# Optimization experiments

Hardware: AMD Instinct MI355X
Metric: run time of the kernel (lower is better)

## Reference

```python
import jax, jax.numpy as jnp
import numpy as np

B, T, C = 4, 2048, 1024


def wkv(k, v, w, u, reverse):
    """RWKV WKV scan with running-max stabilization.
    k, v: [B, T, C]; w, u: [C]. Returns y: [B, T, C]."""
    def step(carry, kv):
        num, den, mx = carry          # each [B, C]
        k_t, v_t = kv                 # each [B, C]
        ku = k_t + u
        m = jnp.maximum(mx, ku)
        e1 = jnp.exp(mx - m)
        e2 = jnp.exp(ku - m)
        y = (e1 * num + e2 * v_t) / (e1 * den + e2)
        # state update with decay w
        mw = mx + w
        mn = jnp.maximum(mw, k_t)
        e1s = jnp.exp(mw - mn)
        e2s = jnp.exp(k_t - mn)
        return (e1s * num + e2s * v_t, e1s * den + e2s, mn), y

    z = jnp.zeros_like(k[:, 0])
    init = (z, z, jnp.full_like(z, -1e38))
    ks = jnp.swapaxes(k, 0, 1)  # [T, B, C]
    vs = jnp.swapaxes(v, 0, 1)
    _, ys = jax.lax.scan(step, init, (ks, vs), reverse=reverse)
    return jnp.swapaxes(ys, 0, 1)


def setup_inputs() -> dict:
    key = jax.random.key(0)
    k1, k2, k3, k4, k5, k6, k7 = jax.random.split(key, 7)
    x = jax.random.normal(k1, (B, T, C), dtype=jnp.float32)
    rkv_w = jax.random.normal(k2, (6 * C, C), dtype=jnp.float32) / np.sqrt(C)
    out_w = jax.random.normal(k3, (C, 2 * C), dtype=jnp.float32) / np.sqrt(2 * C)
    time_decay = jax.random.uniform(k4, (C,), jnp.float32, -6.0, -5.0)
    time_first = jax.random.uniform(k5, (C,), jnp.float32, -3.0, 0.0)
    time_decay_rev = jax.random.uniform(k6, (C,), jnp.float32, -6.0, -5.0)
    time_first_rev = jax.random.uniform(k7, (C,), jnp.float32, -3.0, 0.0)
    return {"x": x, "rkv_w": rkv_w, "out_w": out_w,
            "time_decay": time_decay, "time_first": time_first,
            "time_decay_rev": time_decay_rev, "time_first_rev": time_first_rev}


def reference(x, rkv_w, out_w, time_decay, time_first, time_decay_rev, time_first_rev):
    b, t, c = x.shape
    rkv = jnp.einsum('btc,dc->btd', x, rkv_w).reshape(b, t, 2, 3, c)
    r_f, k_f, v_f = rkv[:, :, 0, 0], rkv[:, :, 0, 1], rkv[:, :, 0, 2]
    r_b, k_b, v_b = rkv[:, :, 1, 0], rkv[:, :, 1, 1], rkv[:, :, 1, 2]
    out_f = jax.nn.sigmoid(r_f) * wkv(k_f, v_f, -jnp.exp(time_decay), time_first, False)
    out_b = jax.nn.sigmoid(r_b) * wkv(k_b, v_b, -jnp.exp(time_decay_rev), time_first_rev, True)
    out_cat = jnp.concatenate([out_f, out_b], axis=-1)  # [B, T, 2C]
    return jnp.einsum('btd,cd->btc', out_cat, out_w)
```

## Files before the change

kernel.cpp:

```cpp
#include <hip/hip_runtime.h>
#include <cstdint>
#include <cstddef>

#define Bdim 4
#define Tdim 2048
#define Cdim 1024

#define SEG  64
#define LSEG (Tdim / SEG)

#define G1_K   1024
#define G1_N   6144
#define G1_NKT 32
#define G1_NWG 1536

typedef __attribute__((ext_vector_type(8))) short bf16x8;
typedef __attribute__((ext_vector_type(4))) float f32x4;

__device__ __forceinline__ unsigned short f2bf(float f) {
    unsigned int u = __float_as_uint(f);
    u += 0x7fffu + ((u >> 16) & 1u);
    return (unsigned short)(u >> 16);
}
__device__ __forceinline__ float bf2f(unsigned short h) {
    return __uint_as_float((unsigned int)h << 16);
}
__device__ __forceinline__ float bf2f_lo(unsigned int u) {
    return __uint_as_float(u << 16);
}
__device__ __forceinline__ float bf2f_hi(unsigned int u) {
    return __uint_as_float(u & 0xffff0000u);
}
__device__ __forceinline__ float frcp(float x) {
    return __builtin_amdgcn_rcpf(x);
}

__device__ __forceinline__ void gload_lds16(const void* g, void* l) {
    __builtin_amdgcn_global_load_lds(
        (const __attribute__((address_space(1))) unsigned int*)g,
        (__attribute__((address_space(3))) unsigned int*)l,
        16, 0, 0);
}

__global__ __launch_bounds__(256) void cast_all(
    const float* __restrict__ x,  unsigned short* __restrict__ xb,  int n1,
    const float* __restrict__ w1, unsigned short* __restrict__ wb,  int n2,
    const float* __restrict__ w2, unsigned short* __restrict__ ob,  int n3)
{
    int i = blockIdx.x * 256 + threadIdx.x;
    const float* in; unsigned short* out;
    if (i < n1)           { in = x;  out = xb; }
    else if (i < n1 + n2) { in = w1; out = wb; i -= n1; }
    else if (i < n1 + n2 + n3) { in = w2; out = ob; i -= n1 + n2; }
    else return;
    float4 v = ((const float4*)in)[i];
    ushort4 o;
    o.x = f2bf(v.x); o.y = f2bf(v.y); o.z = f2bf(v.z); o.w = f2bf(v.w);
    ((ushort4*)out)[i] = o;
}

__device__ __forceinline__ void stage_128(
    const unsigned short* __restrict__ G, int row0, int K, int elemoff,
    char* slot, int wave, int lane)
{
    const int sl = (lane & 3) ^ ((lane >> 3) & 3);
    const unsigned short* gp = G + (size_t)(row0 + wave * 16 + (lane >> 2)) * K
                                 + elemoff + sl * 8;
    gload_lds16(gp, slot + wave * 1024);
}

__global__ __launch_bounds__(512, 4) void gemm1_3slot(
    const unsigned short* __restrict__ A, const unsigned short* __restrict__ B,
    unsigned short* __restrict__ C)
{
    __shared__ char ldsb[73728];

    const int tid  = threadIdx.x;
    const int wave = tid >> 6;
    const int lane = tid & 63;
    const int wm = wave >> 1;
    const int wn = wave & 1;
    const int fr = lane & 15;
    const int cswz = (((lane >> 4) ^ ((fr >> 1) & 3)) << 4);

    const int xcd = blockIdx.x & 7;
    const int li  = blockIdx.x >> 3;
    const int bx  = li >> 2;
    const int by  = xcd * 4 + (li & 3);
    const int m0 = by * 256;
    const int n0 = bx * 128;

    f32x4 acc[4][4] = {};

    stage_128(A, m0,       G1_K, 0,  ldsb + 0,            wave, lane);
    stage_128(A, m0 + 128, G1_K, 0,  ldsb + 8192,         wave, lane);
    stage_128(B, n0,       G1_K, 0,  ldsb + 49152,        wave, lane);
    stage_128(A, m0,       G1_K, 32, ldsb + 16384,        wave, lane);
    stage_128(A, m0 + 128, G1_K, 32, ldsb + 16384 + 8192, wave, lane);
    stage_128(B, n0,       G1_K, 32, ldsb + 49152 + 8192, wave, lane);
    asm volatile("s_waitcnt vmcnt(3)" ::: "memory");
    __builtin_amdgcn_s_barrier();
    __builtin_amdgcn_sched_barrier(0);

    int sR = 0;
    for (int t = 0; t < G1_NKT; ++t) {
        const int sW = (sR >= 1) ? sR - 1 : 2;
        int kst = t + 2; if (kst > G1_NKT - 1) kst = G1_NKT - 1;
        const int keoff = kst * 32;

        const char* Asl = ldsb + sR * 16384;
        const char* Bsl = ldsb + 49152 + sR * 8192;

        bf16x8 af[4], bq[4];
        #pragma unroll
        for (int i_ = 0; i_ < 4; ++i_)
            af[i_] = *(const bf16x8*)(Asl + (wm * 64 + i_ * 16 + fr) * 64 + cswz);
        #pragma unroll
        for (int j_ = 0; j_ < 4; ++j_)
            bq[j_] = *(const bf16x8*)(Bsl + (wn * 64 + j_ * 16 + fr) * 64 + cswz);

        stage_128(A, m0,       G1_K, keoff, ldsb + sW * 16384,        wave, lane);
        stage_128(A, m0 + 128, G1_K, keoff, ldsb + sW * 16384 + 8192, wave, lane);
        stage_128(B, n0,       G1_K, keoff, ldsb + 49152 + sW * 8192, wave, lane);

        __builtin_amdgcn_s_barrier();
        __builtin_amdgcn_sched_barrier(0);
        __builtin_amdgcn_s_setprio(1);
        #pragma unroll
        for (int i_ = 0; i_ < 4; ++i_)
            #pragma unroll
            for (int j_ = 0; j_ < 4; ++j_)
                acc[i_][j_] = __builtin_amdgcn_mfma_f32_16x16x32_bf16(
                    af[i_], bq[j_], acc[i_][j_], 0, 0, 0);
        __builtin_amdgcn_s_setprio(0);
        asm volatile("s_waitcnt vmcnt(3)" ::: "memory");
        __builtin_amdgcn_s_barrier();
        __builtin_amdgcn_sched_barrier(0);

        sR = (sR < 2) ? sR + 1 : 0;
    }

    #pragma unroll
    for (int i_ = 0; i_ < 4; ++i_) {
        const int row = m0 + wm * 64 + i_ * 16 + (lane >> 4) * 4;
        #pragma unroll
        for (int j_ = 0; j_ < 4; ++j_) {
            const int col = n0 + wn * 64 + j_ * 16 + fr;
            #pragma unroll
            for (int r = 0; r < 4; ++r)
                C[(size_t)(row + r) * G1_N + col] = f2bf(acc[i_][j_][r]);
        }
    }
}

__global__ __launch_bounds__(256) void gemm_bf16_nt(
    const unsigned short* __restrict__ A, const unsigned short* __restrict__ B,
    float* __restrict__ C, int M, int N, int K)
{
    __shared__ unsigned short As[128 * 32];
    __shared__ unsigned short Bs[128 * 32];

    const int tid  = threadIdx.x;
    const int wave = tid >> 6;
    const int lane = tid & 63;
    const int m0 = blockIdx.y * 128;
    const int n0 = blockIdx.x * 128;
    const int wr = wave >> 1, wc = wave & 1;

    const int srow = tid >> 2;
    const int scol = (tid & 3) * 8;
    const unsigned short* Ag = A + (size_t)(m0 + srow) * K + scol;
    const unsigned short* Bg = B + (size_t)(n0 + srow) * K + scol;
    char* AsW = (char*)As + wave * 1024;
    char* BsW = (char*)Bs + wave * 1024;

    f32x4 acc[4][4] = {};

    const int fr = lane & 15;
    const int fk = (lane >> 4) * 8;

    for (int k0 = 0; k0 < K; k0 += 32) {
        gload_lds16(Ag + k0,                  AsW);
        gload_lds16(Ag + k0 + (size_t)64 * K, AsW + 4096);
        gload_lds16(Bg + k0,                  BsW);
        gload_lds16(Bg + k0 + (size_t)64 * K, BsW + 4096);
        __syncthreads();

        bf16x8 af[4], bfr_[4];
        #pragma unroll
        for (int f = 0; f < 4; ++f) {
            af[f]   = *(const bf16x8*)&As[(wr * 64 + f * 16 + fr) * 32 + fk];
            bfr_[f] = *(const bf16x8*)&Bs[(wc * 64 + f * 16 + fr) * 32 + fk];
        }
        #pragma unroll
        for (int i = 0; i < 4; ++i)
            #pragma unroll
            for (int j = 0; j < 4; ++j)
                acc[i][j] = __builtin_amdgcn_mfma_f32_16x16x32_bf16(
                    af[i], bfr_[j], acc[i][j], 0, 0, 0);
        __syncthreads();
    }

    #pragma unroll
    for (int i = 0; i < 4; ++i) {
        const int row = m0 + wr * 64 + i * 16 + (lane >> 4) * 4;
        #pragma unroll
        for (int j = 0; j < 4; ++j) {
            const int col = n0 + wc * 64 + j * 16 + (lane & 15);
            #pragma unroll
            for (int r = 0; r < 4; ++r)
                C[(size_t)(row + r) * N + col] = acc[i][j][r];
        }
    }
}

__global__ __launch_bounds__(1024) void wkv_scan_par(
    const unsigned short* __restrict__ rkv,
    const float* __restrict__ td,  const float* __restrict__ tf,
    const float* __restrict__ tdr, const float* __restrict__ tfr,
    unsigned short* __restrict__ outcat)
{
    __shared__ float sBn[SEG][32], sBd[SEG][32], sMb[SEG][32];

    const int tid = threadIdx.x;
    const int chg = tid & 15;
    const int seg = tid >> 4;

    const int bi  = blockIdx.x;
    const int b   = bi >> 6;
    const int rem = bi & 63;
    const int dir = rem >> 5;
    const int cbase = (rem & 31) * 32;
    const int c0  = cbase + chg * 2;

    const float w0 = -__expf(dir ? tdr[c0]     : td[c0]);
    const float w1 = -__expf(dir ? tdr[c0 + 1] : td[c0 + 1]);
    const float u0 = dir ? tfr[c0]     : tf[c0];
    const float u1 = dir ? tfr[c0 + 1] : tf[c0 + 1];

    const int strideT = 6 * Cdim;
    const int tstep   = dir ? -strideT : strideT;
    const int t0      = dir ? (Tdim - 1 - seg * LSEG) : (seg * LSEG);

    const unsigned short* pbase = rkv + ((size_t)b * Tdim + t0) * strideT + dir * 3 * Cdim + c0;

    const int PF = 8;

    float bn0 = 0.f, bd0 = 0.f, mb0 = -1e38f;
    float bn1 = 0.f, bd1 = 0.f, mb1 = -1e38f;
    {
        const unsigned short* q = pbase;
        unsigned int kk[PF], vv[PF];
        #pragma unroll
        for (int i = 0; i < PF; ++i) {
            kk[i] = *(const unsigned int*)(q + Cdim);
            vv[i] = *(const unsigned int*)(q + 2 * Cdim);
            q += tstep;
        }
        for (int t = 0; t < LSEG; t += PF) {
            unsigned int kn[PF], vn[PF];
            if (t + PF < LSEG) {
                #pragma unroll
                for (int i = 0; i < PF; ++i) {
                    kn[i] = *(const unsigned int*)(q + Cdim);
                    vn[i] = *(const unsigned int*)(q + 2 * Cdim);
                    q += tstep;
                }
            }
            #pragma unroll
            for (int i = 0; i < PF; ++i) {
                {
                    const float k_ = bf2f_lo(kk[i]), v_ = bf2f_lo(vv[i]);
                    const float mw = mb0 + w0;
                    const float mn = fmaxf(mw, k_);
                    const float e1 = __expf(mw - mn);
                    const float e2 = __expf(k_ - mn);
                    bn0 = e1 * bn0 + e2 * v_;
                    bd0 = e1 * bd0 + e2;
                    mb0 = mn;
                }
                {
                    const float k_ = bf2f_hi(kk[i]), v_ = bf2f_hi(vv[i]);
                    const float mw = mb1 + w1;
                    const float mn = fmaxf(mw, k_);
                    const float e1 = __expf(mw - mn);
                    const float e2 = __expf(k_ - mn);
                    bn1 = e1 * bn1 + e2 * v_;
                    bd1 = e1 * bd1 + e2;
                    mb1 = mn;
                }
            }
            #pragma unroll
            for (int i = 0; i < PF; ++i) { kk[i] = kn[i]; vv[i] = vn[i]; }
        }
    }
    sBn[seg][chg * 2] = bn0; sBd[seg][chg * 2] = bd0; sMb[seg][chg * 2] = mb0;
    sBn[seg][chg * 2 + 1] = bn1; sBd[seg][chg * 2 + 1] = bd1; sMb[seg][chg * 2 + 1] = mb1;
    __syncthreads();

    if (tid < 32) {
        const float wv = -__expf(dir ? tdr[cbase + tid] : td[cbase + tid]);
        const float a  = wv * (float)LSEG;
        float n = 0.f, d = 0.f, m = -1e38f;
        for (int s = 0; s < SEG; ++s) {
            const float tn = sBn[s][tid], tdn = sBd[s][tid], tm = sMb[s][tid];
            sBn[s][tid] = n; sBd[s][tid] = d; sMb[s][tid] = m;
            const float ma = m + a;
            const float mm = fmaxf(ma, tm);
            const float e1 = __expf(ma - mm);
            const float e2 = __expf(tm - mm);
            n = e1 * n + e2 * tn;
            d = e1 * d + e2 * tdn;
            m = mm;
        }
    }
    __syncthreads();

    float num0 = sBn[seg][chg * 2],     den0 = sBd[seg][chg * 2],     mx0 = sMb[seg][chg * 2];
    float num1 = sBn[seg][chg * 2 + 1], den1 = sBd[seg][chg * 2 + 1], mx1 = sMb[seg][chg * 2 + 1];
    {
        const unsigned short* q = pbase;
        unsigned short* po = outcat + ((size_t)b * Tdim + t0) * (2 * Cdim) + dir * Cdim + c0;
        const int ostep = dir ? -(2 * Cdim) : (2 * Cdim);

        unsigned int rr[PF], kk[PF], vv[PF];
        #pragma unroll
        for (int i = 0; i < PF; ++i) {
            rr[i] = *(const unsigned int*)(q);
            kk[i] = *(const unsigned int*)(q + Cdim);
            vv[i] = *(const unsigned int*)(q + 2 * Cdim);
            q += tstep;
        }
        for (int t = 0; t < LSEG; t += PF) {
            unsigned int rn[PF], kn[PF], vn[PF];
            if (t + PF < LSEG) {
                #pragma unroll
                for (int i = 0; i < PF; ++i) {
                    rn[i] = *(const unsigned int*)(q);
                    kn[i] = *(const unsigned int*)(q + Cdim);
                    vn[i] = *(const unsigned int*)(q + 2 * Cdim);
                    q += tstep;
                }
            }
            #pragma unroll
            for (int i = 0; i < PF; ++i) {
                unsigned int ow;
                {
                    const float k_ = bf2f_lo(kk[i]), v_ = bf2f_lo(vv[i]), r_ = bf2f_lo(rr[i]);
                    const float ku = k_ + u0;
                    const float m  = fmaxf(mx0, ku);
                    const float e1 = __expf(mx0 - m);
                    const float e2 = __expf(ku - m);
                    const float y  = (e1 * num0 + e2 * v_) * frcp(e1 * den0 + e2);
                    const float sr = frcp(1.0f + __expf(-r_));
                    ow = (unsigned int)f2bf(sr * y);
                    const float mw  = mx0 + w0;
                    const float mn  = fmaxf(mw, k_);
                    const float e1s = __expf(mw - mn);
                    const float e2s = __expf(k_ - mn);
                    num0 = e1s * num0 + e2s * v_;
                    den0 = e1s * den0 + e2s;
                    mx0  = mn;
                }
                {
                    const float k_ = bf2f_hi(kk[i]), v_ = bf2f_hi(vv[i]), r_ = bf2f_hi(rr[i]);
                    const float ku = k_ + u1;
                    const float m  = fmaxf(mx1, ku);
                    const float e1 = __expf(mx1 - m);
                    const float e2 = __expf(ku - m);
                    const float y  = (e1 * num1 + e2 * v_) * frcp(e1 * den1 + e2);
                    const float sr = frcp(1.0f + __expf(-r_));
                    ow |= ((unsigned int)f2bf(sr * y)) << 16;
                    const float mw  = mx1 + w1;
                    const float mn  = fmaxf(mw, k_);
                    const float e1s = __expf(mw - mn);
                    const float e2s = __expf(k_ - mn);
                    num1 = e1s * num1 + e2s * v_;
                    den1 = e1s * den1 + e2s;
                    mx1  = mn;
                }
                *(unsigned int*)po = ow;
                po += ostep;
            }
            #pragma unroll
            for (int i = 0; i < PF; ++i) { rr[i] = rn[i]; kk[i] = kn[i]; vv[i] = vn[i]; }
        }
    }
}

extern "C" void kernel_launch(void* const* d_in, const int* in_sizes, int n_in,
                              void* d_out, int out_size, void* d_ws, size_t ws_size,
                              hipStream_t stream)
{
    const float* x    = (const float*)d_in[0];
    const float* rkvw = (const float*)d_in[1];
    const float* outw = (const float*)d_in[2];
    const float* td   = (const float*)d_in[3];
    const float* tf   = (const float*)d_in[4];
    const float* tdr  = (const float*)d_in[5];
    const float* tfr  = (const float*)d_in[6];
    float* out = (float*)d_out;

    const int M = Bdim * Tdim;

    char* ws = (char*)d_ws;
    unsigned short* rkv = (unsigned short*)ws;
    unsigned short* xb  = (unsigned short*)(ws + 100663296);
    unsigned short* wb  = (unsigned short*)(ws + 117440512);
    unsigned short* ob  = (unsigned short*)(ws + 130023424);
    unsigned short* cat = (unsigned short*)(ws + 134217728);

    const int n1 = M * Cdim / 4;
    const int n2 = 6 * Cdim * Cdim / 4;
    const int n3 = Cdim * 2 * Cdim / 4;

    hipLaunchKernelGGL(cast_all, dim3((n1 + n2 + n3 + 255) / 256), dim3(256), 0, stream,
                       x, xb, n1, rkvw, wb, n2, outw, ob, n3);

    hipLaunchKernelGGL(gemm1_3slot, dim3(G1_NWG), dim3(512), 0, stream, xb, wb, rkv);

    hipLaunchKernelGGL(wkv_scan_par, dim3(Bdim * 2 * 32), dim3(1024), 0, stream,
                       rkv, td, tf, tdr, tfr, cat);

    hipLaunchKernelGGL(gemm_bf16_nt, dim3(Cdim / 128, M / 128), dim3(256), 0, stream,
                       cat, ob, out, M, Cdim, 2 * Cdim);
}
```

Baseline: 244.1 us.

## Split WKV scan into three kernels with global segment-state combine

Replaces the single block-local chunked WKV scan with three launches: per-segment summary, a cross-segment combine over global memory, and an emit pass. Each thread now owns two channels of one (batch, dir, segment), so a warp reads 2KB contiguous rows instead of 64-byte slices. The goal is better memory coalescing and removing the serial 32-thread combine that left most of each block idle. The cost is two extra kernel launches, a global round trip for segment states, and a tiny 8-block combine kernel that runs serially over 64 segments.

```diff
diff --git a/kernel.cpp b/kernel.cpp
--- a/kernel.cpp
+++ b/kernel.cpp
@@ -21,9 +21,6 @@
     unsigned int u = __float_as_uint(f);
     u += 0x7fffu + ((u >> 16) & 1u);
     return (unsigned short)(u >> 16);
-}
-__device__ __forceinline__ float bf2f(unsigned short h) {
-    return __uint_as_float((unsigned int)h << 16);
 }
 __device__ __forceinline__ float bf2f_lo(unsigned int u) {
     return __uint_as_float(u << 16);
@@ -214,24 +211,128 @@
     }
 }
 
-__global__ __launch_bounds__(1024) void wkv_scan_par(
+__global__ __launch_bounds__(1024) void wkv_sum(
     const unsigned short* __restrict__ rkv,
     const float* __restrict__ td,  const float* __restrict__ tf,
     const float* __restrict__ tdr, const float* __restrict__ tfr,
+    float* __restrict__ sBn, float* __restrict__ sBd, float* __restrict__ sMb)
+{
+    const int tid  = threadIdx.x;
+    const int lane = tid & 511;
+    const int tup  = tid >> 9;
+    const int tupid = blockIdx.x * 2 + tup;
+    const int b    = tupid >> 7;
+    const int dir  = (tupid >> 6) & 1;
+    const int seg  = tupid & 63;
+    const int c0   = lane * 2;
+
+    const float w0 = -__expf(dir ? tdr[c0]     : td[c0]);
+    const float w1 = -__expf(dir ? tdr[c0 + 1] : td[c0 + 1]);
+
+    const int strideT = 6 * Cdim;
+    const int tstep   = dir ? -strideT : strideT;
+    const int t0      = dir ? (Tdim - 1 - seg * LSEG) : (seg * LSEG);
+
+    const unsigned short* pbase = rkv + ((size_t)b * Tdim + t0) * strideT + dir * 3 * Cdim + c0;
+
+    const int PF = 8;
+    float bn0 = 0.f, bd0 = 0.f, mb0 = -1e38f;
+    float bn1 = 0.f, bd1 = 0.f, mb1 = -1e38f;
+
+    const unsigned short* q = pbase;
+    unsigned int kk[PF], vv[PF];
+    #pragma unroll
+    for (int i = 0; i < PF; ++i) {
+        kk[i] = *(const unsigned int*)(q + Cdim);
+        vv[i] = *(const unsigned int*)(q + 2 * Cdim);
+        q += tstep;
+    }
+    for (int t = 0; t < LSEG; t += PF) {
+        unsigned int kn[PF], vn[PF];
+        if (t + PF < LSEG) {
+            #pragma unroll
+            for (int i = 0; i < PF; ++i) {
+                kn[i] = *(const unsigned int*)(q + Cdim);
+                vn[i] = *(const unsigned int*)(q + 2 * Cdim);
+                q += tstep;
+            }
+        }
+        #pragma unroll
+        for (int i = 0; i < PF; ++i) {
+            {
+                const float k_ = bf2f_lo(kk[i]), v_ = bf2f_lo(vv[i]);
+                const float mw = mb0 + w0;
+                const float mn = fmaxf(mw, k_);
+                const float e1 = __expf(mw - mn);
+                const float e2 = __expf(k_ - mn);
+                bn0 = e1 * bn0 + e2 * v_;
+                bd0 = e1 * bd0 + e2;
+                mb0 = mn;
+            }
+            {
+                const float k_ = bf2f_hi(kk[i]), v_ = bf2f_hi(vv[i]);
+                const float mw = mb1 + w1;
+                const float mn = fmaxf(mw, k_);
+                const float e1 = __expf(mw - mn);
+                const float e2 = __expf(k_ - mn);
+                bn1 = e1 * bn1 + e2 * v_;
+                bd1 = e1 * bd1 + e2;
+                mb1 = mn;
+            }
+        }
+        #pragma unroll
+        for (int i = 0; i < PF; ++i) { kk[i] = kn[i]; vv[i] = vn[i]; }
+    }
+
+    const size_t sidx = (size_t)tupid * Cdim + c0;
+    sBn[sidx] = bn0; sBn[sidx + 1] = bn1;
+    sBd[sidx] = bd0; sBd[sidx + 1] = bd1;
+    sMb[sidx] = mb0; sMb[sidx + 1] = mb1;
+}
+
+__global__ __launch_bounds__(1024) void wkv_comb(
+    const float* __restrict__ td, const float* __restrict__ tdr,
+    float* __restrict__ sBn, float* __restrict__ sBd, float* __restrict__ sMb)
+{
+    const int gid = blockIdx.x * 1024 + threadIdx.x;
+    const int c   = gid & 1023;
+    const int bd  = gid >> 10;
+    const int dir = bd & 1;
+
+    const float wv = -__expf(dir ? tdr[c] : td[c]);
+    const float a  = wv * (float)LSEG;
+
+    float n = 0.f, d = 0.f, m = -1e38f;
+    for (int s = 0; s < SEG; ++s) {
+        const size_t idx = ((size_t)bd * SEG + s) * Cdim + c;
+        const float tn = sBn[idx], tdn = sBd[idx], tm = sMb[idx];
+        sBn[idx] = n; sBd[idx] = d; sMb[idx] = m;
+        const float ma = m + a;
+        const float mm = fmaxf(ma, tm);
+        const float e1 = __expf(ma - mm);
+        const float e2 = __expf(tm - mm);
+        n = e1 * n + e2 * tn;
+        d = e1 * d + e2 * tdn;
+        m = mm;
+    }
+}
+
+__global__ __launch_bounds__(1024) void wkv_emit(
+    const unsigned short* __restrict__ rkv,
+    const float* __restrict__ td,  const float* __restrict__ tf,
+    const float* __restrict__ tdr, const float* __restrict__ tfr,
+    const float* __restrict__ sBn, const float* __restrict__ sBd,
+    const float* __restrict__ sMb,
     unsigned short* __restrict__ outcat)
 {
-    __shared__ float sBn[SEG][32], sBd[SEG][32], sMb[SEG][32];
-
-    const int tid = threadIdx.x;
-    const int chg = tid & 15;
-    const int seg = tid >> 4;
-
-    const int bi  = blockIdx.x;
-    const int b   = bi >> 6;
-    const int rem = bi & 63;
-    const int dir = rem >> 5;
-    const int cbase = (rem & 31) * 32;
-    const int c0  = cbase + chg * 2;
+    const int tid  = threadIdx.x;
+    const int lane = tid & 511;
+    const int tup  = tid >> 9;
+    const int tupid = blockIdx.x * 2 + tup;
+    const int b    = tupid >> 7;
+    const int dir  = (tupid >> 6) & 1;
+    const int seg  = tupid & 63;
+    const int c0   = lane * 2;
 
     const float w0 = -__expf(dir ? tdr[c0]     : td[c0]);
     const float w1 = -__expf(dir ? tdr[c0 + 1] : td[c0 + 1]);
@@ -244,147 +345,76 @@
 
     const unsigned short* pbase = rkv + ((size_t)b * Tdim + t0) * strideT + dir * 3 * Cdim + c0;
 
+    const size_t sidx = (size_t)tupid * Cdim + c0;
+    float num0 = sBn[sidx], den0 = sBd[sidx], mx0 = sMb[sidx];
+    float num1 = sBn[sidx + 1], den1 = sBd[sidx + 1], mx1 = sMb[sidx + 1];
+
+    unsigned short* po = outcat + ((size_t)b * Tdim + t0) * (2 * Cdim) + dir * Cdim + c0;
+    const int ostep = dir ? -(2 * Cdim) : (2 * Cdim);
+
     const int PF = 8;
-
-    float bn0 = 0.f, bd0 = 0.f, mb0 = -1e38f;
-    float bn1 = 0.f, bd1 = 0.f, mb1 = -1e38f;
-    {
-        const unsigned short* q = pbase;
-        unsigned int kk[PF], vv[PF];
+    const unsigned short* q = pbase;
+    unsigned int rr[PF], kk[PF], vv[PF];
+    #pragma unroll
+    for (int i = 0; i < PF; ++i) {
+        rr[i] = *(const unsigned int*)(q);
+        kk[i] = *(const unsigned int*)(q + Cdim);
+        vv[i] = *(const unsigned int*)(q + 2 * Cdim);
+        q += tstep;
+    }
+    for (int t = 0; t < LSEG; t += PF) {
+        unsigned int rn[PF], kn[PF], vn[PF];
+        if (t + PF < LSEG) {
+            #pragma unroll
+            for (int i = 0; i < PF; ++i) {
+                rn[i] = *(const unsigned int*)(q);
+                kn[i] = *(const unsigned int*)(q + Cdim);
+                vn[i] = *(const unsigned int*)(q + 2 * Cdim);
+                q += tstep;
+            }
+        }
         #pragma unroll
         for (int i = 0; i < PF; ++i) {
-            kk[i] = *(const unsigned int*)(q + Cdim);
-            vv[i] = *(const unsigned int*)(q + 2 * Cdim);
-            q += tstep;
-        }
-        for (int t = 0; t < LSEG; t += PF) {
-            unsigned int kn[PF], vn[PF];
-            if (t + PF < LSEG) {
-                #pragma unroll
-                for (int i = 0; i < PF; ++i) {
-                    kn[i] = *(const unsigned int*)(q + Cdim);
-                    vn[i] = *(const unsigned int*)(q + 2 * Cdim);
-                    q += tstep;
-                }
-            }
-            #pragma unroll
-            for (int i = 0; i < PF; ++i) {
-                {
-                    const float k_ = bf2f_lo(kk[i]), v_ = bf2f_lo(vv[i]);
-                    const float mw = mb0 + w0;
-                    const float mn = fmaxf(mw, k_);
-                    const float e1 = __expf(mw - mn);
-                    const float e2 = __expf(k_ - mn);
-                    bn0 = e1 * bn0 + e2 * v_;
-                    bd0 = e1 * bd0 + e2;
-                    mb0 = mn;
-                }
-                {
-                    const float k_ = bf2f_hi(kk[i]), v_ = bf2f_hi(vv[i]);
-                    const float mw = mb1 + w1;
-                    const float mn = fmaxf(mw, k_);
-                    const float e1 = __expf(mw - mn);
-                    const float e2 = __expf(k_ - mn);
-                    bn1 = e1 * bn1 + e2 * v_;
-                    bd1 = e1 * bd1 + e2;
-                    mb1 = mn;
-                }
-            }
-            #pragma unroll
-            for (int i = 0; i < PF; ++i) { kk[i] = kn[i]; vv[i] = vn[i]; }
-        }
-    }
-    sBn[seg][chg * 2] = bn0; sBd[seg][chg * 2] = bd0; sMb[seg][chg * 2] = mb0;
-    sBn[seg][chg * 2 + 1] = bn1; sBd[seg][chg * 2 + 1] = bd1; sMb[seg][chg * 2 + 1] = mb1;
-    __syncthreads();
-
-    if (tid < 32) {
-        const float wv = -__expf(dir ? tdr[cbase + tid] : td[cbase + tid]);
-        const float a  = wv * (float)LSEG;
-        float n = 0.f, d = 0.f, m = -1e38f;
-        for (int s = 0; s < SEG; ++s) {
-            const float tn = sBn[s][tid], tdn = sBd[s][tid], tm = sMb[s][tid];
-            sBn[s][tid] = n; sBd[s][tid] = d; sMb[s][tid] = m;
-            const float ma = m + a;
-            const float mm = fmaxf(ma, tm);
-            const float e1 = __expf(ma - mm);
-            const float e2 = __expf(tm - mm);
-            n = e1 * n + e2 * tn;
-            d = e1 * d + e2 * tdn;
-            m = mm;
-        }
-    }
-    __syncthreads();
-
-    float num0 = sBn[seg][chg * 2],     den0 = sBd[seg][chg * 2],     mx0 = sMb[seg][chg * 2];
-    float num1 = sBn[seg][chg * 2 + 1], den1 = sBd[seg][chg * 2 + 1], mx1 = sMb[seg][chg * 2 + 1];
-    {
-        const unsigned short* q = pbase;
-        unsigned short* po = outcat + ((size_t)b * Tdim + t0) * (2 * Cdim) + dir * Cdim + c0;
-        const int ostep = dir ? -(2 * Cdim) : (2 * Cdim);
-
-        unsigned int rr[PF], kk[PF], vv[PF];
-        #pragma unroll
-        for (int i = 0; i < PF; ++i) {
-            rr[i] = *(const unsigned int*)(q);
-            kk[i] = *(const unsigned int*)(q + Cdim);
-            vv[i] = *(const unsigned int*)(q + 2 * Cdim);
-            q += tstep;
-        }
-        for (int t = 0; t < LSEG; t += PF) {
-            unsigned int rn[PF], kn[PF], vn[PF];
-            if (t + PF < LSEG) {
-                #pragma unroll
-                for (int i = 0; i < PF; ++i) {
-                    rn[i] = *(const unsigned int*)(q);
-                    kn[i] = *(const unsigned int*)(q + Cdim);
-                    vn[i] = *(const unsigned int*)(q + 2 * Cdim);
-                    q += tstep;
-                }
-            }
-            #pragma unroll
-            for (int i = 0; i < PF; ++i) {
-                unsigned int ow;
-                {
-                    const float k_ = bf2f_lo(kk[i]), v_ = bf2f_lo(vv[i]), r_ = bf2f_lo(rr[i]);
-                    const float ku = k_ + u0;
-                    const float m  = fmaxf(mx0, ku);
-                    const float e1 = __expf(mx0 - m);
-                    const float e2 = __expf(ku - m);
-                    const float y  = (e1 * num0 + e2 * v_) * frcp(e1 * den0 + e2);
-                    const float sr = frcp(1.0f + __expf(-r_));
-                    ow = (unsigned int)f2bf(sr * y);
-                    const float mw  = mx0 + w0;
-                    const float mn  = fmaxf(mw, k_);
-                    const float e1s = __expf(mw - mn);
-                    const float e2s = __expf(k_ - mn);
-                    num0 = e1s * num0 + e2s * v_;
-                    den0 = e1s * den0 + e2s;
-                    mx0  = mn;
-                }
-                {
-                    const float k_ = bf2f_hi(kk[i]), v_ = bf2f_hi(vv[i]), r_ = bf2f_hi(rr[i]);
-                    const float ku = k_ + u1;
-                    const float m  = fmaxf(mx1, ku);
-                    const float e1 = __expf(mx1 - m);
-                    const float e2 = __expf(ku - m);
-                    const float y  = (e1 * num1 + e2 * v_) * frcp(e1 * den1 + e2);
-                    const float sr = frcp(1.0f + __expf(-r_));
-                    ow |= ((unsigned int)f2bf(sr * y)) << 16;
-                    const float mw  = mx1 + w1;
-                    const float mn  = fmaxf(mw, k_);
-                    const float e1s = __expf(mw - mn);
-                    const float e2s = __expf(k_ - mn);
-                    num1 = e1s * num1 + e2s * v_;
-                    den1 = e1s * den1 + e2s;
-                    mx1  = mn;
-                }
-                *(unsigned int*)po = ow;
-                po += ostep;
-            }
-            #pragma unroll
-            for (int i = 0; i < PF; ++i) { rr[i] = rn[i]; kk[i] = kn[i]; vv[i] = vn[i]; }
-        }
+            unsigned int ow;
+            {
+                const float k_ = bf2f_lo(kk[i]), v_ = bf2f_lo(vv[i]), r_ = bf2f_lo(rr[i]);
+                const float ku = k_ + u0;
+                const float m  = fmaxf(mx0, ku);
+                const float e1 = __expf(mx0 - m);
+                const float e2 = __expf(ku - m);
+                const float y  = (e1 * num0 + e2 * v_) * frcp(e1 * den0 + e2);
+                const float sr = frcp(1.0f + __expf(-r_));
+                ow = (unsigned int)f2bf(sr * y);
+                const float mw  = mx0 + w0;
+                const float mn  = fmaxf(mw, k_);
+                const float e1s = __expf(mw - mn);
+                const float e2s = __expf(k_ - mn);
+                num0 = e1s * num0 + e2s * v_;
+                den0 = e1s * den0 + e2s;
+                mx0  = mn;
+            }
+            {
+                const float k_ = bf2f_hi(kk[i]), v_ = bf2f_hi(vv[i]), r_ = bf2f_hi(rr[i]);
+                const float ku = k_ + u1;
+                const float m  = fmaxf(mx1, ku);
+                const float e1 = __expf(mx1 - m);
+                const float e2 = __expf(ku - m);
+                const float y  = (e1 * num1 + e2 * v_) * frcp(e1 * den1 + e2);
+                const float sr = frcp(1.0f + __expf(-r_));
+                ow |= ((unsigned int)f2bf(sr * y)) << 16;
+                const float mw  = mx1 + w1;
+                const float mn  = fmaxf(mw, k_);
+                const float e1s = __expf(mw - mn);
+                const float e2s = __expf(k_ - mn);
+                num1 = e1s * num1 + e2s * v_;
+                den1 = e1s * den1 + e2s;
+                mx1  = mn;
+            }
+            *(unsigned int*)po = ow;
+            po += ostep;
+        }
+        #pragma unroll
+        for (int i = 0; i < PF; ++i) { rr[i] = rn[i]; kk[i] = kn[i]; vv[i] = vn[i]; }
     }
 }
 
@@ -409,6 +439,9 @@
     unsigned short* wb  = (unsigned short*)(ws + 117440512);
     unsigned short* ob  = (unsigned short*)(ws + 130023424);
     unsigned short* cat = (unsigned short*)(ws + 134217728);
+    float* sBn = (float*)(ws + 167772160);
+    float* sBd = (float*)(ws + 169869312);
+    float* sMb = (float*)(ws + 171966464);
 
     const int n1 = M * Cdim / 4;
     const int n2 = 6 * Cdim * Cdim / 4;
@@ -419,8 +452,12 @@
 
     hipLaunchKernelGGL(gemm1_3slot, dim3(G1_NWG), dim3(512), 0, stream, xb, wb, rkv);
 
-    hipLaunchKernelGGL(wkv_scan_par, dim3(Bdim * 2 * 32), dim3(1024), 0, stream,
-                       rkv, td, tf, tdr, tfr, cat);
+    hipLaunchKernelGGL(wkv_sum, dim3(256), dim3(1024), 0, stream,
+                       rkv, td, tf, tdr, tfr, sBn, sBd, sMb);
+    hipLaunchKernelGGL(wkv_comb, dim3(8), dim3(1024), 0, stream,
+                       td, tdr, sBn, sBd, sMb);
+    hipLaunchKernelGGL(wkv_emit, dim3(256), dim3(1024), 0, stream,
+                       rkv, td, tf, tdr, tfr, sBn, sBd, sMb, cat);
 
     hipLaunchKernelGGL(gemm_bf16_nt, dim3(Cdim / 128, M / 128), dim3(256), 0, stream,
                        cat, ob, out, M, Cdim, 2 * Cdim);
```

Result: no change. 248.6 us (+1.8%).
